# Performance work log

Hardware: AMD Instinct MI355X
Metric: run time of the kernel (lower is better)

## Reference

```python
import jax, jax.numpy as jnp
import numpy as np

B, S, D, H, F = 8, 1024, 1024, 16, 4096
DH = D // H
EPS = 1e-8
NEG_INF = -1e30


def setup_inputs() -> dict:
    key = jax.random.key(0)
    ks = jax.random.split(key, 12)
    x = jax.random.normal(ks[0], (B, S, D), jnp.float32)
    # variable valid lengths in [S//2, S]; True = keep (valid token)
    lengths = jax.random.randint(ks[1], (B,), S // 2, S + 1)
    src_key_padding_mask = jnp.arange(S)[None, :] < lengths[:, None]
    rel_pos_bias = 0.02 * jax.random.normal(ks[2], (1, H, S, S), jnp.float32)
    w = lambda k, sh, std: std * jax.random.normal(k, sh, jnp.float32)
    std = D ** -0.5
    return {
        'x': x,
        'src_key_padding_mask': src_key_padding_mask,
        'rel_pos_bias': rel_pos_bias,
        'Wq': w(ks[3], (D, D), std),
        'Wk': w(ks[4], (D, D), std),
        'Wv': w(ks[5], (D, D), std),
        'Wo': w(ks[6], (D, D), std),
        'g1': jnp.ones((D,), jnp.float32),
        'g2': jnp.ones((D,), jnp.float32),
        'W1': w(ks[7], (D, F), std),
        'b1': jnp.zeros((F,), jnp.float32),
        'W2': w(ks[8], (F, F and D), F ** -0.5),
        'b2': jnp.zeros((D,), jnp.float32),
    }


def rmsnorm(x, g):
    # x / sqrt(mean(x^2) + eps) * g   (no mean subtraction)
    ms = jnp.mean(x * x, axis=-1, keepdims=True)
    return x * jax.lax.rsqrt(ms + EPS) * g


def attention(h, kpm, rel_pos_bias, Wq, Wk, Wv, Wo):
    b, s, d = h.shape
    q = (h @ Wq).reshape(b, s, H, DH)
    k = (h @ Wk).reshape(b, s, H, DH)
    v = (h @ Wv).reshape(b, s, H, DH)
    scores = jnp.einsum('bqhd,bkhd->bhqk', q, k) / np.sqrt(DH)
    scores = scores + rel_pos_bias
    scores = jnp.where(kpm[:, None, None, :], scores, NEG_INF)
    attn = jax.nn.softmax(scores, axis=-1)
    out = jnp.einsum('bhqk,bkhd->bqhd', attn, v).reshape(b, s, d)
    return out @ Wo


def reference(x, src_key_padding_mask, rel_pos_bias,
              Wq, Wk, Wv, Wo, g1, g2, W1, b1, W2, b2):
    h = rmsnorm(x, g1)
    x = x + attention(h, src_key_padding_mask, rel_pos_bias, Wq, Wk, Wv, Wo)
    h = rmsnorm(x, g2)
    ff = jax.nn.relu(h @ W1 + b1) @ W2 + b2
    return x + ff
```

## Files before the change

kernel.cpp:

```cpp
#include <hip/hip_runtime.h>
#include <stdint.h>

typedef __bf16 bf16;
typedef __bf16 bf16x4 __attribute__((ext_vector_type(4)));
typedef __bf16 bf16x8 __attribute__((ext_vector_type(8)));
typedef float f32x4 __attribute__((ext_vector_type(4)));

constexpr int Bz = 8, S = 1024, D = 1024, NH = 16, DH = 64, F = 4096;

__device__ __forceinline__ bool is_f32(const uint16_t* dt) { return dt[0] == 0; }

__device__ __forceinline__ void ld4(const void* p, size_t idx, bool f32, float o[4]) {
  if (f32) {
    float4 v = *(const float4*)((const float*)p + idx);
    o[0] = v.x; o[1] = v.y; o[2] = v.z; o[3] = v.w;
  } else {
    bf16x4 v = *(const bf16x4*)((const bf16*)p + idx);
    o[0] = v[0]; o[1] = v[1]; o[2] = v[2]; o[3] = v[3];
  }
}

__device__ __forceinline__ float ld1(const void* p, size_t idx, bool f32) {
  return f32 ? ((const float*)p)[idx] : (float)((const bf16*)p)[idx];
}

__device__ __forceinline__ void gload_lds16(const bf16* g, bf16* l) {
  __builtin_amdgcn_global_load_lds(
      (const __attribute__((address_space(1))) void*)g,
      (__attribute__((address_space(3))) void*)l, 16, 0, 0);
}

__global__ void lengths_kernel(const unsigned char* __restrict__ mask,
                               int* __restrict__ lengths) {
  int b = blockIdx.x;
  int esz = (mask[1] == 1) ? 1 : ((mask[1] != 0) ? 2 : 4);
  int cnt = 0;
  for (int s = threadIdx.x; s < S; s += blockDim.x) {
    const unsigned char* p = mask + ((size_t)b * S + s) * esz;
    unsigned v = 0;
    for (int j = 0; j < esz; j++) v |= p[j];
    cnt += (v != 0) ? 1 : 0;
  }
#pragma unroll
  for (int m = 32; m >= 1; m >>= 1) cnt += __shfl_xor(cnt, m);
  __shared__ int sred[4];
  if ((threadIdx.x & 63) == 0) sred[threadIdx.x >> 6] = cnt;
  __syncthreads();
  if (threadIdx.x == 0) lengths[b] = sred[0] + sred[1] + sred[2] + sred[3];
}

__global__ void transpose_any(const void* __restrict__ src, bf16* __restrict__ dst,
                              int R, int C, const uint16_t* __restrict__ dt) {
  bool f32 = is_f32(dt);
  __shared__ bf16 tile[64][65];
  int c0 = blockIdx.x * 64, r0 = blockIdx.y * 64;
  int tx = threadIdx.x, ty = threadIdx.y;
#pragma unroll
  for (int i = 0; i < 4; i++) {
    int r = ty * 4 + i;
    float v[4];
    ld4(src, (size_t)(r0 + r) * C + c0 + tx * 4, f32, v);
#pragma unroll
    for (int j = 0; j < 4; j++) tile[r][tx * 4 + j] = (bf16)v[j];
  }
  __syncthreads();
#pragma unroll
  for (int i = 0; i < 4; i++) {
    int rr = ty * 4 + i;
    bf16x4 ov;
#pragma unroll
    for (int j = 0; j < 4; j++) ov[j] = tile[tx * 4 + j][rr];
    *(bf16x4*)(dst + (size_t)(c0 + rr) * R + r0 + tx * 4) = ov;
  }
}

__global__ void bias_cvt(const void* __restrict__ src, bf16* __restrict__ dst,
                         const uint16_t* __restrict__ dt) {
  bool f32 = is_f32(dt);
  size_t i = ((size_t)blockIdx.x * 256 + threadIdx.x) * 4;
  float v[4];
  ld4(src, i, f32, v);
  bf16x4 o;
#pragma unroll
  for (int j = 0; j < 4; j++) o[j] = (bf16)(v[j] * 1.4426950408889634f);
  *(bf16x4*)(dst + i) = o;
}

template <bool ADD>
__global__ void rmsnorm_kernel(const void* __restrict__ xv, const bf16* __restrict__ add,
                               const void* __restrict__ gv, bf16* __restrict__ y,
                               const uint16_t* __restrict__ dt) {
  bool f32 = is_f32(dt);
  int row = blockIdx.x, t = threadIdx.x;
  float xf[4];
  ld4(xv, (size_t)row * D + t * 4, f32, xf);
  if (ADD) {
    bf16x4 a = *(const bf16x4*)(add + (size_t)row * D + t * 4);
#pragma unroll
    for (int j = 0; j < 4; j++) xf[j] += (float)a[j];
  }
  float ss = xf[0] * xf[0] + xf[1] * xf[1] + xf[2] * xf[2] + xf[3] * xf[3];
#pragma unroll
  for (int m = 32; m >= 1; m >>= 1) ss += __shfl_xor(ss, m);
  __shared__ float sred[4];
  if ((t & 63) == 0) sred[t >> 6] = ss;
  __syncthreads();
  float tot = sred[0] + sred[1] + sred[2] + sred[3];
  float scale = rsqrtf(tot * (1.0f / D) + 1e-8f);
  float gf[4];
  ld4(gv, (size_t)t * 4, f32, gf);
  bf16x4 ov;
#pragma unroll
  for (int j = 0; j < 4; j++) ov[j] = (bf16)(xf[j] * scale * gf[j]);
  *(bf16x4*)(y + (size_t)row * D + t * 4) = ov;
}

template <bool BIAS, bool RELU, bool RES1, bool RES2, bool OUTEXT, bool VT>
__global__ void gemm_nt(const bf16* __restrict__ A, const bf16* __restrict__ Bt,
                        void* __restrict__ Cv, const void* __restrict__ biasv,
                        const void* __restrict__ res1, const bf16* __restrict__ res2,
                        int M, int N, int K, const uint16_t* __restrict__ dt) {
  bool f32 = is_f32(dt);
  __shared__ bf16 As[2 * 4096];
  __shared__ bf16 Bs[2 * 4096];
  const int tid = threadIdx.x, lane = tid & 63, w = tid >> 6;
  const int wm = w >> 1, wn = w & 1;
  const int lid = blockIdx.x;
  const int bm = ((lid & 7) << 3) + ((lid >> 3) & 7);
  const int bn = lid >> 6;
  const int quad = lane >> 4, c = lane & 15;

  f32x4 acc[4][4];
#pragma unroll
  for (int i = 0; i < 4; i++)
#pragma unroll
    for (int j = 0; j < 4; j++)
#pragma unroll
      for (int r = 0; r < 4; r++) acc[i][j][r] = 0.f;

  const bf16* gA = A + (size_t)(bm * 128 + w * 16 + (lane >> 2)) * K + (lane & 3) * 8;
  const bf16* gB = Bt + (size_t)(bn * 128 + w * 16 + (lane >> 2)) * K + (lane & 3) * 8;
  bf16* lA = As + w * 512;
  bf16* lB = Bs + w * 512;
  const size_t rstep = (size_t)64 * K;

  int aoff[4], boff[4];
#pragma unroll
  for (int i = 0; i < 4; i++) {
    aoff[i] = (wm * 64 + i * 16 + c) * 32 + quad * 8;
    boff[i] = (wn * 64 + i * 16 + c) * 32 + quad * 8;
  }

  for (int k0 = 0; k0 < K; k0 += 64) {
    __syncthreads();
#pragma unroll
    for (int p = 0; p < 2; p++) {
      gload_lds16(gA + p * 32, lA + p * 4096);
      gload_lds16(gA + p * 32 + rstep, lA + p * 4096 + 2048);
      gload_lds16(gB + p * 32, lB + p * 4096);
      gload_lds16(gB + p * 32 + rstep, lB + p * 4096 + 2048);
    }
    gA += 64;
    gB += 64;
    __syncthreads();
#pragma unroll
    for (int p = 0; p < 2; p++) {
      bf16x8 af[4], bfr[4];
#pragma unroll
      for (int i = 0; i < 4; i++) af[i] = *(const bf16x8*)(As + p * 4096 + aoff[i]);
#pragma unroll
      for (int i = 0; i < 4; i++) bfr[i] = *(const bf16x8*)(Bs + p * 4096 + boff[i]);
#pragma unroll
      for (int i = 0; i < 4; i++)
#pragma unroll
        for (int j = 0; j < 4; j++)
          acc[i][j] = __builtin_amdgcn_mfma_f32_16x16x32_bf16(af[i], bfr[j], acc[i][j], 0, 0, 0);
    }
  }

  const int m0 = bm * 128 + wm * 64, n0 = bn * 128 + wn * 64;
#pragma unroll
  for (int i = 0; i < 4; i++) {
#pragma unroll
    for (int j = 0; j < 4; j++) {
      int col = n0 + j * 16 + c;
      if (VT) {
        int row0 = m0 + i * 16 + quad * 4;
        int bb = row0 >> 10, s0 = row0 & 1023;
        int hh = col >> 6, dd = col & 63;
        bf16x4 ov;
#pragma unroll
        for (int r = 0; r < 4; r++) ov[r] = (bf16)acc[i][j][r];
        *(bf16x4*)((bf16*)Cv + ((size_t)((bb << 4) + hh) * 64 + dd) * 1024 + s0) = ov;
      } else {
        float bv = BIAS ? ld1(biasv, col, f32) : 0.f;
#pragma unroll
        for (int r = 0; r < 4; r++) {
          int row = m0 + i * 16 + quad * 4 + r;
          size_t idx = (size_t)row * N + col;
          float vv = acc[i][j][r] + bv;
          if (RELU) vv = fmaxf(vv, 0.f);
          if (RES1) vv += ld1(res1, idx, f32);
          if (RES2) vv += (float)res2[idx];
          if (OUTEXT && f32) ((float*)Cv)[idx] = vv;
          else ((bf16*)Cv)[idx] = (bf16)vv;
        }
      }
    }
  }
}

__global__ void __launch_bounds__(256) attn_kernel(
    const bf16* __restrict__ qk, const bf16* __restrict__ vt,
    const bf16* __restrict__ bias, const int* __restrict__ lengths,
    bf16* __restrict__ out) {
  __shared__ bf16 QPs[64 * 72];
  __shared__ bf16 Ks[64][72];
  __shared__ bf16 Vs[64][72];
  const int tid = threadIdx.x, lane = tid & 63, w = tid >> 6;
  const int id = blockIdx.x;
  const int qt = id >> 7, b = (id >> 4) & 7, h = id & 15;
  const int len = lengths[b];
  const int quad = lane >> 4, c = lane & 15;
  const int r4 = tid >> 2, c4 = tid & 3;

  {
    size_t qrow = (size_t)(b * S + qt * 64 + r4) * 2048 + h * 64 + c4 * 8;
    *(bf16x8*)&QPs[r4 * 72 + c4 * 8] = *(const bf16x8*)&qk[qrow];
    *(bf16x8*)&QPs[r4 * 72 + 32 + c4 * 8] = *(const bf16x8*)&qk[qrow + 32];
  }
  __syncthreads();
  const bf16x8 a0 = *(const bf16x8*)&QPs[(w * 16 + c) * 72 + quad * 8];
  const bf16x8 a1 = *(const bf16x8*)&QPs[(w * 16 + c) * 72 + 32 + quad * 8];

  bf16* Pw = QPs + w * 16 * 72;
  const int xsw = (quad & 2) << 3;
  const int xsr = (c & 8) << 1;

  float l_[4] = {0.f, 0.f, 0.f, 0.f};
  f32x4 o[4];
#pragma unroll
  for (int ni = 0; ni < 4; ni++)
#pragma unroll
    for (int r = 0; r < 4; r++) o[ni][r] = 0.f;

  const bf16* bbp = bias + (size_t)h * S * S + (size_t)(qt * 64 + w * 16 + quad * 4) * S;
  const int nkt = (len + 63) >> 6;

  const size_t KSTEP = (size_t)64 * 2048;
  const bf16* gk = qk + (size_t)(b * S + r4) * 2048 + 1024 + h * 64 + c4 * 8;
  const bf16* gv = vt + ((size_t)((b * 16 + h) * 64 + r4)) * 1024 + c4 * 8;
  bf16x8 kr0 = *(const bf16x8*)gk;
  bf16x8 kr1 = *(const bf16x8*)(gk + 32);
  bf16x8 vr0 = *(const bf16x8*)gv;
  bf16x8 vr1 = *(const bf16x8*)(gv + 32);
  gk += KSTEP;
  gv += 64;

  for (int kt = 0; kt < nkt; kt++) {
    __syncthreads();
    *(bf16x8*)&Ks[r4][c4 * 8] = kr0;
    *(bf16x8*)&Ks[r4][32 + c4 * 8] = kr1;
    *(bf16x8*)&Vs[r4][c4 * 8] = vr0;
    *(bf16x8*)&Vs[r4][32 + c4 * 8] = vr1;
    __syncthreads();

    bf16 br[4][4];
#pragma unroll
    for (int ni = 0; ni < 4; ni++)
#pragma unroll
      for (int r = 0; r < 4; r++) br[ni][r] = bbp[(size_t)r * S + ni * 16 + c];

    if (kt + 1 < nkt) {
      kr0 = *(const bf16x8*)gk;
      kr1 = *(const bf16x8*)(gk + 32);
      vr0 = *(const bf16x8*)gv;
      vr1 = *(const bf16x8*)(gv + 32);
      gk += KSTEP;
      gv += 64;
    }

    f32x4 s[4];
#pragma unroll
    for (int ni = 0; ni < 4; ni++)
#pragma unroll
      for (int r = 0; r < 4; r++) s[ni][r] = 0.f;
#pragma unroll
    for (int ni = 0; ni < 4; ni++) {
      bf16x8 b0 = *(const bf16x8*)&Ks[ni * 16 + c][quad * 8];
      bf16x8 b1 = *(const bf16x8*)&Ks[ni * 16 + c][32 + quad * 8];
      s[ni] = __builtin_amdgcn_mfma_f32_16x16x32_bf16(a0, b0, s[ni], 0, 0, 0);
      s[ni] = __builtin_amdgcn_mfma_f32_16x16x32_bf16(a1, b1, s[ni], 0, 0, 0);
    }

    const bool full = (kt * 64 + 64 <= len);
#pragma unroll
    for (int ni = 0; ni < 4; ni++) {
      int col = kt * 64 + ni * 16 + c;
      bool valid = full || (col < len);
#pragma unroll
      for (int r = 0; r < 4; r++) {
        float p = valid ? exp2f(fmaf(s[ni][r], 0.18033688011112042f, (float)br[ni][r])) : 0.f;
        s[ni][r] = p;
        l_[r] += p;
      }
    }

#pragma unroll
    for (int ni = 0; ni < 4; ni++)
#pragma unroll
      for (int r = 0; r < 4; r++)
        Pw[(quad * 4 + r) * 72 + ((ni * 16 + c) ^ xsw)] = (bf16)s[ni][r];

    bf16x8 p0 = *(const bf16x8*)&Pw[c * 72 + ((quad * 8) ^ xsr)];
    bf16x8 p1 = *(const bf16x8*)&Pw[c * 72 + ((32 + quad * 8) ^ xsr)];
#pragma unroll
    for (int ni = 0; ni < 4; ni++) {
      bf16x8 vb0 = *(const bf16x8*)&Vs[ni * 16 + c][quad * 8];
      bf16x8 vb1 = *(const bf16x8*)&Vs[ni * 16 + c][32 + quad * 8];
      o[ni] = __builtin_amdgcn_mfma_f32_16x16x32_bf16(p0, vb0, o[ni], 0, 0, 0);
      o[ni] = __builtin_amdgcn_mfma_f32_16x16x32_bf16(p1, vb1, o[ni], 0, 0, 0);
    }
    bbp += 64;
  }

  float inv[4];
#pragma unroll
  for (int r = 0; r < 4; r++) {
    float l = l_[r];
    l += __shfl_xor(l, 1);
    l += __shfl_xor(l, 2);
    l += __shfl_xor(l, 4);
    l += __shfl_xor(l, 8);
    inv[r] = 1.f / l;
  }
#pragma unroll
  for (int ni = 0; ni < 4; ni++)
#pragma unroll
    for (int r = 0; r < 4; r++) {
      size_t idx = ((size_t)(b * S + qt * 64 + w * 16 + quad * 4 + r)) * D + h * 64 + ni * 16 + c;
      out[idx] = (bf16)(o[ni][r] * inv[r]);
    }
}

extern "C" void kernel_launch(void* const* d_in, const int* in_sizes, int n_in,
                              void* d_out, int out_size, void* d_ws, size_t ws_size,
                              hipStream_t stream) {
  const void* x = d_in[0];
  const unsigned char* mask = (const unsigned char*)d_in[1];
  const void* rpb = d_in[2];
  const void* Wq = d_in[3];
  const void* Wk = d_in[4];
  const void* Wv = d_in[5];
  const void* Wo = d_in[6];
  const void* g1 = d_in[7];
  const void* g2 = d_in[8];
  const void* W1 = d_in[9];
  const void* b1 = d_in[10];
  const void* W2 = d_in[11];
  const void* b2 = d_in[12];
  const uint16_t* dt = (const uint16_t*)d_in[7];

  char* ws = (char*)d_ws;
  const size_t MB = 1024 * 1024;
  bf16* WqkT = (bf16*)(ws + 0 * MB);
  bf16* WkT = (bf16*)(ws + 2 * MB);
  bf16* WvT = (bf16*)(ws + 4 * MB);
  bf16* WoT = (bf16*)(ws + 6 * MB);
  bf16* W1T = (bf16*)(ws + 8 * MB);
  bf16* W2T = (bf16*)(ws + 16 * MB);
  bf16* hbuf = (bf16*)(ws + 24 * MB);
  bf16* qkbuf = (bf16*)(ws + 40 * MB);
  bf16* d1buf = (bf16*)(ws + 40 * MB);
  bf16* vtbuf = (bf16*)(ws + 72 * MB);
  bf16* biasb = (bf16*)(ws + 88 * MB);
  bf16* a1b = (bf16*)(ws + 56 * MB);
  int* lens = (int*)d_out;

  dim3 tb(16, 16);
  lengths_kernel<<<dim3(8), dim3(256), 0, stream>>>(mask, lens);
  transpose_any<<<dim3(16, 16), tb, 0, stream>>>(Wq, WqkT, 1024, 1024, dt);
  transpose_any<<<dim3(16, 16), tb, 0, stream>>>(Wk, WkT, 1024, 1024, dt);
  transpose_any<<<dim3(16, 16), tb, 0, stream>>>(Wv, WvT, 1024, 1024, dt);
  transpose_any<<<dim3(16, 16), tb, 0, stream>>>(Wo, WoT, 1024, 1024, dt);
  transpose_any<<<dim3(64, 16), tb, 0, stream>>>(W1, W1T, 1024, 4096, dt);
  transpose_any<<<dim3(16, 64), tb, 0, stream>>>(W2, W2T, 4096, 1024, dt);
  bias_cvt<<<dim3(16384), dim3(256), 0, stream>>>(rpb, biasb, dt);

  rmsnorm_kernel<false><<<dim3(8192), dim3(256), 0, stream>>>(x, nullptr, g1, hbuf, dt);
  gemm_nt<false, false, false, false, false, false><<<dim3(16 * 64), dim3(256), 0, stream>>>(
      hbuf, WqkT, qkbuf, nullptr, nullptr, nullptr, 8192, 2048, 1024, dt);
  gemm_nt<false, false, false, false, false, true><<<dim3(8 * 64), dim3(256), 0, stream>>>(
      hbuf, WvT, vtbuf, nullptr, nullptr, nullptr, 8192, 1024, 1024, dt);
  attn_kernel<<<dim3(2048), dim3(256), 0, stream>>>(qkbuf, vtbuf, biasb, lens, hbuf);
  gemm_nt<false, false, false, false, false, false><<<dim3(8 * 64), dim3(256), 0, stream>>>(
      hbuf, WoT, d1buf, nullptr, nullptr, nullptr, 8192, 1024, 1024, dt);
  rmsnorm_kernel<true><<<dim3(8192), dim3(256), 0, stream>>>(x, d1buf, g2, hbuf, dt);
  gemm_nt<true, true, false, false, false, false><<<dim3(32 * 64), dim3(256), 0, stream>>>(
      hbuf, W1T, a1b, b1, nullptr, nullptr, 8192, 4096, 1024, dt);
  gemm_nt<true, false, true, true, true, false><<<dim3(8 * 64), dim3(256), 0, stream>>>(
      a1b, W2T, d_out, b2, x, d1buf, 8192, 1024, 4096, dt);

  (void)in_sizes; (void)n_in; (void)out_size; (void)ws_size;
}
```

Baseline: 550.0 us.

## Add 256x256-tile pipelined GEMM for QK projection and FFN up-projection

Adds a new 512-thread GEMM kernel with 256x256 output tiles, double-buffered LDS filled by direct global-to-LDS loads, XOR-swizzled shared layout, and a four-phase interleaved schedule with barriers and wave priority bumps. It replaces the generic gemm_nt for the fused Q/K projection and the W1+bias+ReLU GEMM. The larger tiles raise arithmetic intensity and the staged prefetch overlaps memory with MFMA work. In exchange it uses much more LDS and registers per block, and yields fewer blocks (256 and 512), which may leave the GPU underfilled or expose tail effects.

```diff
diff --git a/kernel.cpp b/kernel.cpp
--- a/kernel.cpp
+++ b/kernel.cpp
@@ -208,6 +208,158 @@
       }
     }
   }
+}
+
+#define SYNC()                            \
+  do {                                    \
+    __builtin_amdgcn_sched_barrier(0);    \
+    __builtin_amdgcn_s_barrier();         \
+    __builtin_amdgcn_sched_barrier(0);    \
+  } while (0)
+#define VMW(n)                                              \
+  do {                                                      \
+    asm volatile("s_waitcnt vmcnt(" #n ")" ::: "memory");   \
+    __builtin_amdgcn_sched_barrier(0);                      \
+  } while (0)
+#define STA_(nb, rowbase, kb)                                                  \
+  do {                                                                         \
+    gload_lds16(Ag + (size_t)(rowbase) * K + (kb), &Abuf[nb][(rowbase) * 64]); \
+    gload_lds16(Ag + (size_t)((rowbase) + 8) * K + (kb),                       \
+                &Abuf[nb][((rowbase) + 8) * 64]);                              \
+  } while (0)
+#define STB_(nb, rowbase, kb)                                                  \
+  do {                                                                         \
+    gload_lds16(Bg + (size_t)(rowbase) * K + (kb), &Bbuf[nb][(rowbase) * 64]); \
+    gload_lds16(Bg + (size_t)((rowbase) + 8) * K + (kb),                       \
+                &Bbuf[nb][((rowbase) + 8) * 64]);                              \
+  } while (0)
+#define RDA_(MQ, fr, bufsel)                                                        \
+  do {                                                                              \
+    _Pragma("unroll") for (int ii = 0; ii < 4; ii++) {                              \
+      int arow = wm * 128 + ((MQ)*4 + ii) * 16 + c;                                 \
+      fr[ii][0] = *(const bf16x8*)&Abuf[bufsel][arow * 64 + ((quad ^ sx) * 8)];     \
+      fr[ii][1] = *(const bf16x8*)&Abuf[bufsel][arow * 64 + (((4 + quad) ^ sx) * 8)]; \
+    }                                                                               \
+  } while (0)
+#define RDB_(NQ, fr, bufsel)                                                        \
+  do {                                                                              \
+    _Pragma("unroll") for (int jj = 0; jj < 2; jj++) {                              \
+      int brow = wn * 64 + ((NQ)*2 + jj) * 16 + c;                                  \
+      fr[jj][0] = *(const bf16x8*)&Bbuf[bufsel][brow * 64 + ((quad ^ sx) * 8)];     \
+      fr[jj][1] = *(const bf16x8*)&Bbuf[bufsel][brow * 64 + (((4 + quad) ^ sx) * 8)]; \
+    }                                                                               \
+  } while (0)
+
+template <int MQ, int NQ>
+__device__ __forceinline__ void mm_phase(f32x4 (&acc)[8][4], const bf16x8 (&afr)[4][2],
+                                         const bf16x8 (&bfr)[2][2]) {
+#pragma unroll
+  for (int ii = 0; ii < 4; ii++)
+#pragma unroll
+    for (int jj = 0; jj < 2; jj++) {
+      acc[MQ * 4 + ii][NQ * 2 + jj] = __builtin_amdgcn_mfma_f32_16x16x32_bf16(
+          afr[ii][0], bfr[jj][0], acc[MQ * 4 + ii][NQ * 2 + jj], 0, 0, 0);
+      acc[MQ * 4 + ii][NQ * 2 + jj] = __builtin_amdgcn_mfma_f32_16x16x32_bf16(
+          afr[ii][1], bfr[jj][1], acc[MQ * 4 + ii][NQ * 2 + jj], 0, 0, 0);
+    }
+}
+
+template <bool BIAS, bool RELU>
+__global__ void __launch_bounds__(512, 2) gemm256(
+    const bf16* __restrict__ A, const bf16* __restrict__ Bt, bf16* __restrict__ C,
+    const void* __restrict__ biasv, int N, int K, const uint16_t* __restrict__ dt) {
+  bool f32 = is_f32(dt);
+  __shared__ bf16 Abuf[2][256 * 64];
+  __shared__ bf16 Bbuf[2][256 * 64];
+  const int tid = threadIdx.x, lane = tid & 63, w = tid >> 6;
+  const int wm = w >> 2, wn = w & 3;
+  const int quad = lane >> 4, c = lane & 15;
+  const int sx = c & 7;
+  const int nbn = N >> 8;
+  const int nwg = gridDim.x;
+  const int sid = (blockIdx.x & 7) * (nwg >> 3) + (blockIdx.x >> 3);
+  const int bm = sid / nbn, bn = sid % nbn;
+
+  const int lrow = lane >> 3;
+  const int lslot = ((lane & 7) ^ lrow) * 8;
+  const bf16* Ag = A + (size_t)(bm * 256 + lrow) * K + lslot;
+  const bf16* Bg = Bt + (size_t)(bn * 256 + lrow) * K + lslot;
+
+  const int ra0 = wm * 128 + wn * 16;
+  const int ra1 = ra0 + 64;
+  const int rb0 = (wn >> 1) * 128 + (wn & 1) * 64 + wm * 16;
+  const int rb1 = rb0 + 32;
+
+  f32x4 acc[8][4];
+#pragma unroll
+  for (int i = 0; i < 8; i++)
+#pragma unroll
+    for (int j = 0; j < 4; j++)
+#pragma unroll
+      for (int r = 0; r < 4; r++) acc[i][j][r] = 0.f;
+
+  const int nt = K >> 6;
+
+  STA_(0, ra0, 0);
+  STA_(0, ra1, 0);
+  STB_(0, rb0, 0);
+  STB_(0, rb1, 0);
+  STA_(1, ra0, 64);
+  VMW(2);
+  SYNC();
+
+  for (int t = 0; t < nt; ++t) {
+    const int buf = t & 1, nb = buf ^ 1;
+    const int kb1 = (t + 1) << 6, kb2 = (t + 2) << 6;
+    const bool st1 = (t + 1 < nt), st2 = (t + 2 < nt);
+    bf16x8 afr[4][2], bfr0[2][2], bfr1[2][2];
+    RDA_(0, afr, buf);
+    RDB_(0, bfr0, buf);
+    if (st1) STA_(nb, ra1, kb1);
+    SYNC();
+    __builtin_amdgcn_s_setprio(1);
+    mm_phase<0, 0>(acc, afr, bfr0);
+    __builtin_amdgcn_s_setprio(0);
+    VMW(2);
+    SYNC();
+    RDB_(1, bfr1, buf);
+    if (st1) STB_(nb, rb0, kb1);
+    SYNC();
+    __builtin_amdgcn_s_setprio(1);
+    mm_phase<0, 1>(acc, afr, bfr1);
+    __builtin_amdgcn_s_setprio(0);
+    SYNC();
+    RDA_(1, afr, buf);
+    if (st2) STA_(buf, ra0, kb2);
+    SYNC();
+    __builtin_amdgcn_s_setprio(1);
+    mm_phase<1, 0>(acc, afr, bfr0);
+    __builtin_amdgcn_s_setprio(0);
+    SYNC();
+    if (st1) STB_(nb, rb1, kb1);
+    SYNC();
+    __builtin_amdgcn_s_setprio(1);
+    mm_phase<1, 1>(acc, afr, bfr1);
+    __builtin_amdgcn_s_setprio(0);
+    VMW(4);
+    SYNC();
+  }
+
+  const int m0 = bm * 256 + wm * 128, n0 = bn * 256 + wn * 64;
+#pragma unroll
+  for (int fi = 0; fi < 8; fi++)
+#pragma unroll
+    for (int fj = 0; fj < 4; fj++) {
+      int col = n0 + fj * 16 + c;
+      float bv = BIAS ? ld1(biasv, col, f32) : 0.f;
+#pragma unroll
+      for (int r = 0; r < 4; r++) {
+        int row = m0 + fi * 16 + quad * 4 + r;
+        float vv = acc[fi][fj][r] + bv;
+        if (RELU) vv = fmaxf(vv, 0.f);
+        C[(size_t)row * N + col] = (bf16)vv;
+      }
+    }
 }
 
 __global__ void __launch_bounds__(256) attn_kernel(
@@ -388,16 +540,16 @@
   bias_cvt<<<dim3(16384), dim3(256), 0, stream>>>(rpb, biasb, dt);
 
   rmsnorm_kernel<false><<<dim3(8192), dim3(256), 0, stream>>>(x, nullptr, g1, hbuf, dt);
-  gemm_nt<false, false, false, false, false, false><<<dim3(16 * 64), dim3(256), 0, stream>>>(
-      hbuf, WqkT, qkbuf, nullptr, nullptr, nullptr, 8192, 2048, 1024, dt);
+  gemm256<false, false><<<dim3(256), dim3(512), 0, stream>>>(
+      hbuf, WqkT, qkbuf, nullptr, 2048, 1024, dt);
   gemm_nt<false, false, false, false, false, true><<<dim3(8 * 64), dim3(256), 0, stream>>>(
       hbuf, WvT, vtbuf, nullptr, nullptr, nullptr, 8192, 1024, 1024, dt);
   attn_kernel<<<dim3(2048), dim3(256), 0, stream>>>(qkbuf, vtbuf, biasb, lens, hbuf);
   gemm_nt<false, false, false, false, false, false><<<dim3(8 * 64), dim3(256), 0, stream>>>(
       hbuf, WoT, d1buf, nullptr, nullptr, nullptr, 8192, 1024, 1024, dt);
   rmsnorm_kernel<true><<<dim3(8192), dim3(256), 0, stream>>>(x, d1buf, g2, hbuf, dt);
-  gemm_nt<true, true, false, false, false, false><<<dim3(32 * 64), dim3(256), 0, stream>>>(
-      hbuf, W1T, a1b, b1, nullptr, nullptr, 8192, 4096, 1024, dt);
+  gemm256<true, true><<<dim3(512), dim3(512), 0, stream>>>(
+      hbuf, W1T, a1b, b1, 4096, 1024, dt);
   gemm_nt<true, false, true, true, true, false><<<dim3(8 * 64), dim3(256), 0, stream>>>(
       a1b, W2T, d_out, b2, x, d1buf, 8192, 1024, 4096, dt);
 
```

Measured after the change: 547.5 us. Within noise of the previous version (-0.5%).

## Fuse weight transposes and bias conversion into one launch; remap GEMM tiles per XCD

Applied to the files above, without the earlier changes.

Six weight-transpose launches and the relative-position-bias conversion kernel are merged into a single prep kernel that dispatches on block index, removing seven launch gaps and tail idle time. Separately, the GEMM block-to-tile mapping is changed so that consecutive block IDs on the same XCD (lid & 7) share a contiguous range of N tiles. The intent is better L2 reuse of B-matrix columns per chiplet. The new mapping assumes N/128 is divisible by 8, which holds for every N launched here.

```diff
diff --git a/kernel.cpp b/kernel.cpp
--- a/kernel.cpp
+++ b/kernel.cpp
@@ -49,12 +49,44 @@
   if (threadIdx.x == 0) lengths[b] = sred[0] + sred[1] + sred[2] + sred[3];
 }
 
-__global__ void transpose_any(const void* __restrict__ src, bf16* __restrict__ dst,
-                              int R, int C, const uint16_t* __restrict__ dt) {
+__global__ void prep_all(const void* __restrict__ sq, const void* __restrict__ sk,
+                         const void* __restrict__ sv, const void* __restrict__ so,
+                         const void* __restrict__ s1, const void* __restrict__ s2,
+                         bf16* __restrict__ dq, bf16* __restrict__ dk,
+                         bf16* __restrict__ dv, bf16* __restrict__ do_,
+                         bf16* __restrict__ d1, bf16* __restrict__ d2,
+                         const void* __restrict__ rpb, bf16* __restrict__ biasb,
+                         const uint16_t* __restrict__ dt) {
   bool f32 = is_f32(dt);
+  int t = blockIdx.x;
+  int tx = threadIdx.x, ty = threadIdx.y;
+  if (t >= 3072) {
+    size_t i = ((size_t)(t - 3072) * 256 + ty * 16 + tx) * 4;
+    float v[4];
+    ld4(rpb, i, f32, v);
+    bf16x4 o;
+#pragma unroll
+    for (int j = 0; j < 4; j++) o[j] = (bf16)(v[j] * 1.4426950408889634f);
+    *(bf16x4*)(biasb + i) = o;
+    return;
+  }
+  const void* src;
+  bf16* dst;
+  int R, C, gx, base;
+  if (t < 1024) {
+    int wsel = t >> 8;
+    base = wsel << 8;
+    src = wsel == 0 ? sq : wsel == 1 ? sk : wsel == 2 ? sv : so;
+    dst = wsel == 0 ? dq : wsel == 1 ? dk : wsel == 2 ? dv : do_;
+    R = 1024; C = 1024; gx = 16;
+  } else if (t < 2048) {
+    base = 1024; src = s1; dst = d1; R = 1024; C = 4096; gx = 64;
+  } else {
+    base = 2048; src = s2; dst = d2; R = 4096; C = 1024; gx = 16;
+  }
+  int rel = t - base;
+  int c0 = (rel % gx) * 64, r0 = (rel / gx) * 64;
   __shared__ bf16 tile[64][65];
-  int c0 = blockIdx.x * 64, r0 = blockIdx.y * 64;
-  int tx = threadIdx.x, ty = threadIdx.y;
 #pragma unroll
   for (int i = 0; i < 4; i++) {
     int r = ty * 4 + i;
@@ -72,18 +104,6 @@
     for (int j = 0; j < 4; j++) ov[j] = tile[tx * 4 + j][rr];
     *(bf16x4*)(dst + (size_t)(c0 + rr) * R + r0 + tx * 4) = ov;
   }
-}
-
-__global__ void bias_cvt(const void* __restrict__ src, bf16* __restrict__ dst,
-                         const uint16_t* __restrict__ dt) {
-  bool f32 = is_f32(dt);
-  size_t i = ((size_t)blockIdx.x * 256 + threadIdx.x) * 4;
-  float v[4];
-  ld4(src, i, f32, v);
-  bf16x4 o;
-#pragma unroll
-  for (int j = 0; j < 4; j++) o[j] = (bf16)(v[j] * 1.4426950408889634f);
-  *(bf16x4*)(dst + i) = o;
 }
 
 template <bool ADD>
@@ -126,8 +146,12 @@
   const int tid = threadIdx.x, lane = tid & 63, w = tid >> 6;
   const int wm = w >> 1, wn = w & 1;
   const int lid = blockIdx.x;
-  const int bm = ((lid & 7) << 3) + ((lid >> 3) & 7);
-  const int bn = lid >> 6;
+  const int nbn = N >> 7;
+  const int nbn8 = nbn >> 3;
+  const int xcd = lid & 7;
+  const int rr2 = lid >> 3;
+  const int bn = xcd * nbn8 + (rr2 % nbn8);
+  const int bm = rr2 / nbn8;
   const int quad = lane >> 4, c = lane & 15;
 
   f32x4 acc[4][4];
@@ -377,15 +401,9 @@
   bf16* a1b = (bf16*)(ws + 56 * MB);
   int* lens = (int*)d_out;
 
-  dim3 tb(16, 16);
   lengths_kernel<<<dim3(8), dim3(256), 0, stream>>>(mask, lens);
-  transpose_any<<<dim3(16, 16), tb, 0, stream>>>(Wq, WqkT, 1024, 1024, dt);
-  transpose_any<<<dim3(16, 16), tb, 0, stream>>>(Wk, WkT, 1024, 1024, dt);
-  transpose_any<<<dim3(16, 16), tb, 0, stream>>>(Wv, WvT, 1024, 1024, dt);
-  transpose_any<<<dim3(16, 16), tb, 0, stream>>>(Wo, WoT, 1024, 1024, dt);
-  transpose_any<<<dim3(64, 16), tb, 0, stream>>>(W1, W1T, 1024, 4096, dt);
-  transpose_any<<<dim3(16, 64), tb, 0, stream>>>(W2, W2T, 4096, 1024, dt);
-  bias_cvt<<<dim3(16384), dim3(256), 0, stream>>>(rpb, biasb, dt);
+  prep_all<<<dim3(3072 + 16384), dim3(16, 16), 0, stream>>>(
+      Wq, Wk, Wv, Wo, W1, W2, WqkT, WkT, WvT, WoT, W1T, W2T, rpb, biasb, dt);
 
   rmsnorm_kernel<false><<<dim3(8192), dim3(256), 0, stream>>>(x, nullptr, g1, hbuf, dt);
   gemm_nt<false, false, false, false, false, false><<<dim3(16 * 64), dim3(256), 0, stream>>>(
```

Result: no change. 553.7 us (+0.7%).
